# Performance work log

Measured on AMD Instinct MI355X. Metric: run time of the kernel, lower is better.

Reference implementation:

```python
import jax, jax.numpy as jnp
import numpy as np

BLOCK = 256      # fixed sequence length (causal mask size)
N_EMBD = 384
N_HEAD = 6
HEAD = N_EMBD // N_HEAD  # 64
LN_EPS = 1e-5
B = 512


def setup_inputs() -> dict:
    key = jax.random.key(0)
    k0, k1, k2 = jax.random.split(key, 3)
    logits = jax.random.normal(k0, (B, BLOCK, N_EMBD), dtype=jnp.float32)
    ln_gamma = jnp.ones((N_EMBD,), jnp.float32)
    ln_beta = jnp.zeros((N_EMBD,), jnp.float32)
    # per-head fused QKV weight: (H, E, 3*HEAD), bias-free like nn.Linear(N_EMBD, 3*HEAD, bias=False)
    w_qkv = jax.random.normal(k1, (N_HEAD, N_EMBD, 3 * HEAD), dtype=jnp.float32) * 0.02
    w_proj = jax.random.normal(k2, (N_EMBD, N_EMBD), dtype=jnp.float32) * 0.02
    b_proj = jnp.zeros((N_EMBD,), jnp.float32)
    return {"logits": logits, "ln_gamma": ln_gamma, "ln_beta": ln_beta,
            "w_qkv": w_qkv, "w_proj": w_proj, "b_proj": b_proj}


def reference(logits, ln_gamma, ln_beta, w_qkv, w_proj, b_proj):
    # LayerNorm over last dim (applied BEFORE attention, as in the torch module)
    mu = jnp.mean(logits, axis=-1, keepdims=True)
    var = jnp.mean(jnp.square(logits - mu), axis=-1, keepdims=True)
    x = (logits - mu) * jax.lax.rsqrt(var + LN_EPS) * ln_gamma + ln_beta

    # fused per-head QKV projection: (B,S,E) x (H,E,3d) -> (B,H,S,3d)
    qkv = jnp.einsum('bse,hed->bhsd', x, w_qkv)
    q, k, v = jnp.split(qkv, 3, axis=-1)  # each (B,H,S,HEAD)

    scale = HEAD ** -0.5
    scores = jnp.einsum('bhqd,bhkd->bhqk', q, k) * scale  # (B,H,S,S)
    causal = jnp.tril(jnp.ones((BLOCK, BLOCK), dtype=bool))
    scores = jnp.where(causal, scores, -jnp.inf)
    attn = jax.nn.softmax(scores, axis=-1)

    out = jnp.einsum('bhqk,bhkd->bhqd', attn, v)          # (B,H,S,HEAD)
    out = out.transpose(0, 2, 1, 3).reshape(B, BLOCK, N_EMBD)  # concat heads
    return out @ w_proj + b_proj
```

## Files before the change

### kernel.cpp

```cpp
#include <hip/hip_runtime.h>

typedef __attribute__((ext_vector_type(8))) short bf16x8;
typedef __attribute__((ext_vector_type(4))) float f32x4;
typedef __attribute__((ext_vector_type(4))) unsigned int u32x4;
typedef __attribute__((ext_vector_type(2))) unsigned int u32x2;
typedef unsigned short u16;
typedef unsigned int u32;

__device__ __forceinline__ u16 f2bf(float f) {
    union { float f; u32 u; } c; c.f = f;
    return (u16)((c.u + 0x7FFFu + ((c.u >> 16) & 1u)) >> 16);
}

__device__ __forceinline__ bf16x8 ld16(const void* p) {
    union { uint4 u; bf16x8 v; } c;
    c.u = *reinterpret_cast<const uint4*>(p);
    return c.v;
}

__device__ __forceinline__ u32 cvtpk(float lo, float hi) {
    u32 r;
    asm("v_cvt_pk_bf16_f32 %0, %1, %2" : "=v"(r) : "v"(lo), "v"(hi));
    return r;
}

__global__ void prep_kernel(const float* __restrict__ wqkv, const float* __restrict__ wproj,
                            u16* __restrict__ Wqt, u16* __restrict__ Wpt) {
    int idx = blockIdx.x * 256 + threadIdx.x;
    if (idx < 6 * 192 * 384) {
        int k = idx % 384;
        int n = idx / 384;
        int h = n / 192, dd = n % 192;
        Wqt[idx] = f2bf(wqkv[(h * 384 + k) * 192 + dd]);
    }
    if (idx < 384 * 384) {
        int k = idx % 384, n = idx / 384;
        Wpt[idx] = f2bf(wproj[k * 384 + n]);
    }
}

__global__ __launch_bounds__(256) void ln_kernel(const float* __restrict__ x,
                                                 const float* __restrict__ gamma,
                                                 const float* __restrict__ beta,
                                                 u16* __restrict__ xln) {
    int row = blockIdx.x * 4 + (threadIdx.x >> 6);
    int l = threadIdx.x & 63;
    const float* xr = x + (size_t)row * 384;
    float2 v[3];
    float s = 0.f, sq = 0.f;
#pragma unroll
    for (int i = 0; i < 3; ++i) {
        v[i] = *reinterpret_cast<const float2*>(xr + i * 128 + l * 2);
        s += v[i].x + v[i].y;
        sq += v[i].x * v[i].x + v[i].y * v[i].y;
    }
#pragma unroll
    for (int m = 1; m < 64; m <<= 1) {
        s += __shfl_xor(s, m, 64);
        sq += __shfl_xor(sq, m, 64);
    }
    float mean = s * (1.0f / 384.0f);
    float var = sq * (1.0f / 384.0f) - mean * mean;
    float rstd = rsqrtf(var + 1e-5f);
#pragma unroll
    for (int i = 0; i < 3; ++i) {
        int c = i * 128 + l * 2;
        float y0 = (v[i].x - mean) * rstd * gamma[c] + beta[c];
        float y1 = (v[i].y - mean) * rstd * gamma[c + 1] + beta[c + 1];
        u32 packed = (u32)f2bf(y0) | ((u32)f2bf(y1) << 16);
        *reinterpret_cast<u32*>(xln + (size_t)row * 384 + c) = packed;
    }
}

__global__ __launch_bounds__(256, 3) void qkv_kernel(const u16* __restrict__ xln,
                                                     const u16* __restrict__ Wqt,
                                                     u16* __restrict__ qkvout) {
    __shared__ u16 As[2][128 * 32];
    __shared__ u16 Bs[2][192 * 32];
    const int mt = blockIdx.x;
    const int h = blockIdx.y;
    const int t = threadIdx.x;
    const int l = t & 63, w = t >> 6;
    const int wm = w >> 1, wn = w & 1;
    const int l15 = l & 15, lq = l >> 4;
    const int rloc = l >> 2;
    const int m0 = mt * 128;
    const u16* Ag = xln + (size_t)m0 * 384;
    const u16* Bg = Wqt + (size_t)h * 192 * 384;
    f32x4 acc[4][6];
#pragma unroll
    for (int rg = 0; rg < 4; ++rg)
#pragma unroll
        for (int cg = 0; cg < 6; ++cg) acc[rg][cg] = (f32x4){0.f, 0.f, 0.f, 0.f};

    auto stage = [&](int kt, int buf) {
#pragma unroll
        for (int i = 0; i < 2; ++i) {
            int row = w * 32 + i * 16 + rloc;
            int ss = (l & 3) ^ ((row >> 1) & 3);
            __builtin_amdgcn_global_load_lds(Ag + (size_t)row * 384 + kt * 32 + ss * 8,
                                             &As[buf][(w * 32 + i * 16) * 32], 16, 0, 0);
        }
#pragma unroll
        for (int i = 0; i < 3; ++i) {
            int row = w * 48 + i * 16 + rloc;
            int ss = (l & 3) ^ ((row >> 1) & 3);
            __builtin_amdgcn_global_load_lds(Bg + (size_t)row * 384 + kt * 32 + ss * 8,
                                             &Bs[buf][(w * 48 + i * 16) * 32], 16, 0, 0);
        }
    };

    stage(0, 0);
    __syncthreads();

    for (int kt = 0; kt < 12; ++kt) {
        const int cur = kt & 1;
        if (kt < 11) stage(kt + 1, cur ^ 1);
        char* Ab = reinterpret_cast<char*>(As[cur]);
        char* Bb = reinterpret_cast<char*>(Bs[cur]);
        bf16x8 af[4], bf[6];
#pragma unroll
        for (int rg = 0; rg < 4; ++rg) {
            int row = wm * 64 + rg * 16 + l15;
            af[rg] = ld16(Ab + row * 64 + ((lq ^ ((row >> 1) & 3)) << 4));
        }
#pragma unroll
        for (int cg = 0; cg < 6; ++cg) {
            int row = wn * 96 + cg * 16 + l15;
            bf[cg] = ld16(Bb + row * 64 + ((lq ^ ((row >> 1) & 3)) << 4));
        }
#pragma unroll
        for (int rg = 0; rg < 4; ++rg)
#pragma unroll
            for (int cg = 0; cg < 6; ++cg)
                acc[rg][cg] = __builtin_amdgcn_mfma_f32_16x16x32_bf16(af[rg], bf[cg], acc[rg][cg], 0, 0, 0);
        __syncthreads();
    }
    const int b = m0 >> 8;
    const int s0 = m0 & 255;
    u16* out = qkvout + ((size_t)(b * 6 + h) * 256) * 192;
#pragma unroll
    for (int rg = 0; rg < 4; ++rg)
#pragma unroll
        for (int cg = 0; cg < 6; ++cg)
#pragma unroll
            for (int r = 0; r < 4; ++r) {
                int s = s0 + wm * 64 + rg * 16 + lq * 4 + r;
                int dd = wn * 96 + cg * 16 + l15;
                out[(size_t)s * 192 + dd] = f2bf(acc[rg][cg][r]);
            }
}

__global__ __launch_bounds__(512, 2) void attn_kernel(const u16* __restrict__ qkv,
                                                      u16* __restrict__ aout) {
    __shared__ u16 Ks[256 * 64];
    __shared__ u16 Vt[64 * 256];
    __shared__ u16 Ps[8 * 16 * 32];
    const int bh = blockIdx.x;
    const int b = bh / 6, h = bh % 6;
    const u16* base = qkv + (size_t)bh * (256 * 192);
    const int t = threadIdx.x;
    const int w = t >> 6, l = t & 63;
    const int l15 = l & 15, lq = l >> 4;

#pragma unroll
    for (int i = 0; i < 4; ++i) {
        int u = t + 512 * i;
        int row = u >> 3, seg = u & 7;
        uint4 v = *reinterpret_cast<const uint4*>(base + row * 192 + 64 + seg * 8);
        *reinterpret_cast<uint4*>(reinterpret_cast<char*>(Ks) + row * 128 + ((seg * 16) ^ ((row & 7) << 4))) = v;
    }
    {
        int j = t >> 1, d0 = (t & 1) * 32;
#pragma unroll
        for (int c = 0; c < 4; ++c) {
            uint4 v = *reinterpret_cast<const uint4*>(base + j * 192 + 128 + d0 + c * 8);
            const u16* pv = reinterpret_cast<const u16*>(&v);
#pragma unroll
            for (int e = 0; e < 8; ++e) {
                int d = d0 + c * 8 + e;
                *reinterpret_cast<u16*>(reinterpret_cast<char*>(Vt) + d * 512 + ((j * 2) ^ ((d & 7) << 4))) = pv[e];
            }
        }
    }
    const int qrow0 = w * 16;
    const int qrow1 = (15 - w) * 16;
    const int kbmax0 = w >> 2;
    const int kbmax1 = (15 - w) >> 2;
    bf16x8 qf[2][2];
#pragma unroll
    for (int kk = 0; kk < 2; ++kk) {
        qf[0][kk] = ld16(base + (qrow0 + l15) * 192 + kk * 32 + lq * 8);
        qf[1][kk] = ld16(base + (qrow1 + l15) * 192 + kk * 32 + lq * 8);
    }
    __syncthreads();

    f32x4 acc[2][4];
#pragma unroll
    for (int rg = 0; rg < 2; ++rg)
#pragma unroll
        for (int dg = 0; dg < 4; ++dg) acc[rg][dg] = (f32x4){0.f, 0.f, 0.f, 0.f};
    float l_r[2] = {0.f, 0.f};

    const float CEXP = 0.18033688011112042f;
    char* pbase = reinterpret_cast<char*>(Ps) + w * 1024;
    auto fs = [](int row) { return ((row + (row >> 2)) & 3) << 4; };
    const int myfs = fs(l15);

    for (int kb = 0; kb <= kbmax1; ++kb) {
        const bool do0 = (kb <= kbmax0);
        f32x4 sc[2][4];
#pragma unroll
        for (int rg = 0; rg < 2; ++rg)
#pragma unroll
            for (int cg = 0; cg < 4; ++cg) sc[rg][cg] = (f32x4){0.f, 0.f, 0.f, 0.f};
#pragma unroll
        for (int kk = 0; kk < 2; ++kk) {
            bf16x8 kf[4];
#pragma unroll
            for (int cg = 0; cg < 4; ++cg) {
                int krow = kb * 64 + cg * 16 + l15;
                kf[cg] = ld16(reinterpret_cast<char*>(Ks) + krow * 128 + ((kk * 64 + lq * 16) ^ ((krow & 7) << 4)));
            }
            if (do0)
#pragma unroll
                for (int cg = 0; cg < 4; ++cg)
                    sc[0][cg] = __builtin_amdgcn_mfma_f32_16x16x32_bf16(kf[cg], qf[0][kk], sc[0][cg], 0, 0, 0);
#pragma unroll
            for (int cg = 0; cg < 4; ++cg)
                sc[1][cg] = __builtin_amdgcn_mfma_f32_16x16x32_bf16(kf[cg], qf[1][kk], sc[1][cg], 0, 0, 0);
        }
#pragma unroll
        for (int rg = 0; rg < 2; ++rg) {
            if (rg == 0 && !do0) continue;
            const int qb = rg ? qrow1 : qrow0;
            const int diag = rg ? kbmax1 : kbmax0;
            if (kb == diag) {
                int gq = qb + l15;
#pragma unroll
                for (int cg = 0; cg < 4; ++cg)
#pragma unroll
                    for (int r = 0; r < 4; ++r) {
                        int gk = kb * 64 + cg * 16 + lq * 4 + r;
                        if (gk > gq) sc[rg][cg][r] = -3.0e38f;
                    }
            }
#pragma unroll
            for (int cg = 0; cg < 4; ++cg)
#pragma unroll
                for (int r = 0; r < 4; ++r)
                    sc[rg][cg][r] = exp2f(sc[rg][cg][r] * CEXP);
            float s = ((sc[rg][0][0] + sc[rg][0][1]) + (sc[rg][0][2] + sc[rg][0][3]))
                    + ((sc[rg][1][0] + sc[rg][1][1]) + (sc[rg][1][2] + sc[rg][1][3]))
                    + ((sc[rg][2][0] + sc[rg][2][1]) + (sc[rg][2][2] + sc[rg][2][3]))
                    + ((sc[rg][3][0] + sc[rg][3][1]) + (sc[rg][3][2] + sc[rg][3][3]));
            s += __shfl_xor(s, 16, 64);
            s += __shfl_xor(s, 32, 64);
            l_r[rg] += s;
            u32 pk0[4], pk1[4];
#pragma unroll
            for (int cg = 0; cg < 4; ++cg) {
                pk0[cg] = cvtpk(sc[rg][cg][0], sc[rg][cg][1]);
                pk1[cg] = cvtpk(sc[rg][cg][2], sc[rg][cg][3]);
            }
#pragma unroll
            for (int kk = 0; kk < 2; ++kk) {
#pragma unroll
                for (int c2 = 0; c2 < 2; ++c2) {
                    int cg = kk * 2 + c2;
                    u32x2 wv;
                    wv.x = pk0[cg];
                    wv.y = pk1[cg];
                    *reinterpret_cast<u32x2*>(pbase + l15 * 64 + ((c2 * 32 + lq * 8) ^ myfs)) = wv;
                }
                bf16x8 pf = ld16(pbase + l15 * 64 + ((lq * 16) ^ myfs));
                bf16x8 vf[4];
#pragma unroll
                for (int dg = 0; dg < 4; ++dg) {
                    int d = dg * 16 + l15;
                    vf[dg] = ld16(reinterpret_cast<char*>(Vt) + d * 512 + ((kb * 128 + kk * 64 + lq * 16) ^ ((d & 7) << 4)));
                }
#pragma unroll
                for (int dg = 0; dg < 4; ++dg)
                    acc[rg][dg] = __builtin_amdgcn_mfma_f32_16x16x32_bf16(pf, vf[dg], acc[rg][dg], 0, 0, 0);
            }
        }
    }
#pragma unroll
    for (int rg = 0; rg < 2; ++rg) {
        const int qb = rg ? qrow1 : qrow0;
#pragma unroll
        for (int r = 0; r < 4; ++r) {
            float lr = __shfl(l_r[rg], lq * 4 + r, 64);
            float inv = 1.0f / lr;
            int gq = qb + lq * 4 + r;
            u16* orow = aout + ((size_t)b * 256 + gq) * 384 + h * 64;
#pragma unroll
            for (int dg = 0; dg < 4; ++dg) orow[dg * 16 + l15] = f2bf(acc[rg][dg][r] * inv);
        }
    }
}

__global__ __launch_bounds__(256, 2) void proj_kernel(const u16* __restrict__ A,
                                                      const u16* __restrict__ Wpt,
                                                      const float* __restrict__ bias,
                                                      float* __restrict__ out) {
    __shared__ u16 S[32768];
    u16* Asb[2] = {S, S + 8192};
    u16* Bsb[2] = {S + 16384, S + 24576};
    const int mt = blockIdx.x;
    const int nt = blockIdx.y;
    const int t = threadIdx.x;
    const int l = t & 63, w = t >> 6;
    const int wm = w >> 1, wn = w & 1;
    const int l15 = l & 15, lq = l >> 4;
    const int rloc = l >> 3, seg = l & 7;
    const int m0 = mt * 128;
    const u16* Ag = A + (size_t)m0 * 384;
    const u16* Bg = Wpt + (size_t)nt * 128 * 384;
    f32x4 acc[4][4];
#pragma unroll
    for (int rg = 0; rg < 4; ++rg)
#pragma unroll
        for (int cg = 0; cg < 4; ++cg) acc[rg][cg] = (f32x4){0.f, 0.f, 0.f, 0.f};

    auto stage = [&](int kt, int buf) {
#pragma unroll
        for (int i = 0; i < 4; ++i) {
            int row = w * 32 + i * 8 + rloc;
            int ss = seg ^ (row & 7);
            __builtin_amdgcn_global_load_lds(Ag + (size_t)row * 384 + kt * 64 + ss * 8,
                                             &Asb[buf][(w * 32 + i * 8) * 64], 16, 0, 0);
            __builtin_amdgcn_global_load_lds(Bg + (size_t)row * 384 + kt * 64 + ss * 8,
                                             &Bsb[buf][(w * 32 + i * 8) * 64], 16, 0, 0);
        }
    };

    stage(0, 0);
    __syncthreads();

    for (int kt = 0; kt < 6; ++kt) {
        const int cur = kt & 1;
        if (kt < 5) stage(kt + 1, cur ^ 1);
        char* Ab = reinterpret_cast<char*>(Asb[cur]);
        char* Bb = reinterpret_cast<char*>(Bsb[cur]);
        bf16x8 af[4][2], bf[4][2];
#pragma unroll
        for (int rg = 0; rg < 4; ++rg)
#pragma unroll
            for (int kk = 0; kk < 2; ++kk) {
                int row = wm * 64 + rg * 16 + l15;
                af[rg][kk] = ld16(Ab + row * 128 + ((kk * 64 + lq * 16) ^ ((row & 7) << 4)));
            }
#pragma unroll
        for (int cg = 0; cg < 4; ++cg)
#pragma unroll
            for (int kk = 0; kk < 2; ++kk) {
                int row = wn * 64 + cg * 16 + l15;
                bf[cg][kk] = ld16(Bb + row * 128 + ((kk * 64 + lq * 16) ^ ((row & 7) << 4)));
            }
#pragma unroll
        for (int kk = 0; kk < 2; ++kk)
#pragma unroll
            for (int rg = 0; rg < 4; ++rg)
#pragma unroll
                for (int cg = 0; cg < 4; ++cg)
                    acc[rg][cg] = __builtin_amdgcn_mfma_f32_16x16x32_bf16(af[rg][kk], bf[cg][kk], acc[rg][cg], 0, 0, 0);
        __syncthreads();
    }
    float* ftile = reinterpret_cast<float*>(S);
#pragma unroll
    for (int rg = 0; rg < 4; ++rg)
#pragma unroll
        for (int cg = 0; cg < 4; ++cg) {
            int n_loc = wn * 64 + cg * 16 + l15;
            float bv = bias[nt * 128 + n_loc];
#pragma unroll
            for (int r = 0; r < 4; ++r) {
                int m_loc = wm * 64 + rg * 16 + lq * 4 + r;
                ftile[m_loc * 128 + n_loc] = acc[rg][cg][r] + bv;
            }
        }
    __syncthreads();
    float* outp = out + (size_t)m0 * 384 + nt * 128;
#pragma unroll
    for (int i = 0; i < 16; ++i) {
        int idx = t + 256 * i;
        int row = idx >> 5;
        int c = (idx & 31) * 4;
        u32x4 v = *reinterpret_cast<const u32x4*>(ftile + row * 128 + c);
        __builtin_nontemporal_store(v, reinterpret_cast<u32x4*>(outp + (size_t)row * 384 + c));
    }
}

extern "C" void kernel_launch(void* const* d_in, const int* in_sizes, int n_in,
                              void* d_out, int out_size, void* d_ws, size_t ws_size,
                              hipStream_t stream) {
    const float* logits = (const float*)d_in[0];
    const float* gamma  = (const float*)d_in[1];
    const float* beta   = (const float*)d_in[2];
    const float* wqkv   = (const float*)d_in[3];
    const float* wproj  = (const float*)d_in[4];
    const float* bproj  = (const float*)d_in[5];
    float* out = (float*)d_out;

    char* ws = (char*)d_ws;
    u16* Wqt  = (u16*)(ws);
    u16* Wpt  = (u16*)(ws + 884736);
    u16* xln  = (u16*)(ws + 1179648);
    u16* qkvb = (u16*)(ws + 101842944);
    u16* attnout = xln;

    hipLaunchKernelGGL(prep_kernel, dim3(1728), dim3(256), 0, stream, wqkv, wproj, Wqt, Wpt);
    hipLaunchKernelGGL(ln_kernel, dim3(32768), dim3(256), 0, stream, logits, gamma, beta, xln);
    hipLaunchKernelGGL(qkv_kernel, dim3(1024, 6), dim3(256), 0, stream, xln, Wqt, qkvb);
    hipLaunchKernelGGL(attn_kernel, dim3(3072), dim3(512), 0, stream, qkvb, attnout);
    hipLaunchKernelGGL(proj_kernel, dim3(1024, 3), dim3(256), 0, stream, attnout, Wpt, bproj, out);
}
```

Baseline: 402.5 us.

## Widen QKV GEMM tile to two heads per block and hoist V loads in attention

```diff
diff --git a/kernel.cpp b/kernel.cpp
--- a/kernel.cpp
+++ b/kernel.cpp
@@ -72,21 +72,21 @@
     }
 }
 
-__global__ __launch_bounds__(256, 3) void qkv_kernel(const u16* __restrict__ xln,
+__global__ __launch_bounds__(512, 2) void qkv_kernel(const u16* __restrict__ xln,
                                                      const u16* __restrict__ Wqt,
                                                      u16* __restrict__ qkvout) {
     __shared__ u16 As[2][128 * 32];
-    __shared__ u16 Bs[2][192 * 32];
+    __shared__ u16 Bs[2][384 * 32];
     const int mt = blockIdx.x;
-    const int h = blockIdx.y;
+    const int nt = blockIdx.y;
     const int t = threadIdx.x;
     const int l = t & 63, w = t >> 6;
-    const int wm = w >> 1, wn = w & 1;
+    const int wm = w >> 2, wn = w & 3;
     const int l15 = l & 15, lq = l >> 4;
     const int rloc = l >> 2;
     const int m0 = mt * 128;
     const u16* Ag = xln + (size_t)m0 * 384;
-    const u16* Bg = Wqt + (size_t)h * 192 * 384;
+    const u16* Bg = Wqt + (size_t)nt * 384 * 384;
     f32x4 acc[4][6];
 #pragma unroll
     for (int rg = 0; rg < 4; ++rg)
@@ -94,12 +94,11 @@
         for (int cg = 0; cg < 6; ++cg) acc[rg][cg] = (f32x4){0.f, 0.f, 0.f, 0.f};
 
     auto stage = [&](int kt, int buf) {
-#pragma unroll
-        for (int i = 0; i < 2; ++i) {
-            int row = w * 32 + i * 16 + rloc;
+        {
+            int row = w * 16 + rloc;
             int ss = (l & 3) ^ ((row >> 1) & 3);
             __builtin_amdgcn_global_load_lds(Ag + (size_t)row * 384 + kt * 32 + ss * 8,
-                                             &As[buf][(w * 32 + i * 16) * 32], 16, 0, 0);
+                                             &As[buf][(w * 16) * 32], 16, 0, 0);
         }
 #pragma unroll
         for (int i = 0; i < 3; ++i) {
@@ -138,15 +137,16 @@
     }
     const int b = m0 >> 8;
     const int s0 = m0 & 255;
-    u16* out = qkvout + ((size_t)(b * 6 + h) * 256) * 192;
+    const int h = nt * 2 + (wn >> 1);
+    u16* out = qkvout + ((size_t)(b * 6 + h) * 256 + s0) * 192;
 #pragma unroll
     for (int rg = 0; rg < 4; ++rg)
 #pragma unroll
         for (int cg = 0; cg < 6; ++cg)
 #pragma unroll
             for (int r = 0; r < 4; ++r) {
-                int s = s0 + wm * 64 + rg * 16 + lq * 4 + r;
-                int dd = wn * 96 + cg * 16 + l15;
+                int s = wm * 64 + rg * 16 + lq * 4 + r;
+                int dd = (wn & 1) * 96 + cg * 16 + l15;
                 out[(size_t)s * 192 + dd] = f2bf(acc[rg][cg][r]);
             }
 }
@@ -230,6 +230,7 @@
             for (int cg = 0; cg < 4; ++cg)
                 sc[1][cg] = __builtin_amdgcn_mfma_f32_16x16x32_bf16(kf[cg], qf[1][kk], sc[1][cg], 0, 0, 0);
         }
+        u32 pk0[2][4], pk1[2][4];
 #pragma unroll
         for (int rg = 0; rg < 2; ++rg) {
             if (rg == 0 && !do0) continue;
@@ -257,29 +258,32 @@
             s += __shfl_xor(s, 16, 64);
             s += __shfl_xor(s, 32, 64);
             l_r[rg] += s;
-            u32 pk0[4], pk1[4];
 #pragma unroll
             for (int cg = 0; cg < 4; ++cg) {
-                pk0[cg] = cvtpk(sc[rg][cg][0], sc[rg][cg][1]);
-                pk1[cg] = cvtpk(sc[rg][cg][2], sc[rg][cg][3]);
-            }
-#pragma unroll
-            for (int kk = 0; kk < 2; ++kk) {
+                pk0[rg][cg] = cvtpk(sc[rg][cg][0], sc[rg][cg][1]);
+                pk1[rg][cg] = cvtpk(sc[rg][cg][2], sc[rg][cg][3]);
+            }
+        }
+#pragma unroll
+        for (int kk = 0; kk < 2; ++kk) {
+            bf16x8 vf[4];
+#pragma unroll
+            for (int dg = 0; dg < 4; ++dg) {
+                int d = dg * 16 + l15;
+                vf[dg] = ld16(reinterpret_cast<char*>(Vt) + d * 512 + ((kb * 128 + kk * 64 + lq * 16) ^ ((d & 7) << 4)));
+            }
+#pragma unroll
+            for (int rg = 0; rg < 2; ++rg) {
+                if (rg == 0 && !do0) continue;
 #pragma unroll
                 for (int c2 = 0; c2 < 2; ++c2) {
                     int cg = kk * 2 + c2;
                     u32x2 wv;
-                    wv.x = pk0[cg];
-                    wv.y = pk1[cg];
+                    wv.x = pk0[rg][cg];
+                    wv.y = pk1[rg][cg];
                     *reinterpret_cast<u32x2*>(pbase + l15 * 64 + ((c2 * 32 + lq * 8) ^ myfs)) = wv;
                 }
                 bf16x8 pf = ld16(pbase + l15 * 64 + ((lq * 16) ^ myfs));
-                bf16x8 vf[4];
-#pragma unroll
-                for (int dg = 0; dg < 4; ++dg) {
-                    int d = dg * 16 + l15;
-                    vf[dg] = ld16(reinterpret_cast<char*>(Vt) + d * 512 + ((kb * 128 + kk * 64 + lq * 16) ^ ((d & 7) << 4)));
-                }
 #pragma unroll
                 for (int dg = 0; dg < 4; ++dg)
                     acc[rg][dg] = __builtin_amdgcn_mfma_f32_16x16x32_bf16(pf, vf[dg], acc[rg][dg], 0, 0, 0);
@@ -413,7 +417,7 @@
 
     hipLaunchKernelGGL(prep_kernel, dim3(1728), dim3(256), 0, stream, wqkv, wproj, Wqt, Wpt);
     hipLaunchKernelGGL(ln_kernel, dim3(32768), dim3(256), 0, stream, logits, gamma, beta, xln);
-    hipLaunchKernelGGL(qkv_kernel, dim3(1024, 6), dim3(256), 0, stream, xln, Wqt, qkvb);
+    hipLaunchKernelGGL(qkv_kernel, dim3(1024, 3), dim3(512), 0, stream, xln, Wqt, qkvb);
     hipLaunchKernelGGL(attn_kernel, dim3(3072), dim3(512), 0, stream, qkvb, attnout);
     hipLaunchKernelGGL(proj_kernel, dim3(1024, 3), dim3(256), 0, stream, attnout, Wpt, bproj, out);
 }
```

New measurement: 454.7 us. +13.0%, slower.
